# Kernel tuning notes

Hardware: AMD Instinct MI355X
Metric: run time of the kernel (lower is better)

## Reference

```python
import jax, jax.numpy as jnp
import numpy as np

EMBED_DIM = 1024
NUM_HEADS = 16
HEAD_DIM = EMBED_DIM // NUM_HEADS


def setup_inputs() -> dict:
    key = jax.random.key(0)
    ks = jax.random.split(key, 10)
    B, T, E = 2, 2048, EMBED_DIM

    def xavier(k, shape):
        fan_in, fan_out = shape[1], shape[0]
        limit = (6.0 / (fan_in + fan_out)) ** 0.5
        return jax.random.uniform(k, shape, jnp.float32, -limit, limit)

    return {
        "query": jax.random.normal(ks[0], (B, T, E), jnp.float32),
        "key": jax.random.normal(ks[1], (B, T, E), jnp.float32),
        "value": jax.random.normal(ks[2], (B, T, E), jnp.float32),
        "Wq": xavier(ks[3], (E, E)),
        "Wk": xavier(ks[4], (E, E)),
        "Wv": xavier(ks[5], (E, E)),
        "bq": jnp.zeros((E,), jnp.float32),
        "bk": jnp.zeros((E,), jnp.float32),
        "bv": jnp.zeros((E,), jnp.float32),
        "Wo": xavier(ks[6], (E, E)),
        "bo": jnp.zeros((E,), jnp.float32),
    }


def reference(query, key, value, Wq, Wk, Wv, bq, bk, bv, Wo, bo):
    B, Tq, E = query.shape
    Tk = key.shape[1]
    H, hd = NUM_HEADS, HEAD_DIM

    # In-projections (nn.Linear convention: x @ W.T + b)
    q = query @ Wq.T + bq  # (B, Tq, E)
    k = key @ Wk.T + bk    # (B, Tk, E)
    v = value @ Wv.T + bv  # (B, Tk, E)

    # Split heads -> (B, H, T, hd)
    q = q.reshape(B, Tq, H, hd).transpose(0, 2, 1, 3)
    k = k.reshape(B, Tk, H, hd).transpose(0, 2, 1, 3)
    v = v.reshape(B, Tk, H, hd).transpose(0, 2, 1, 3)

    # Scaled dot-product attention (dropout=0, no mask)
    scores = jnp.einsum("bhqd,bhkd->bhqk", q, k) / jnp.sqrt(jnp.float32(hd))
    attn = jax.nn.softmax(scores, axis=-1)
    out = jnp.einsum("bhqk,bhkd->bhqd", attn, v)  # (B, H, Tq, hd)

    # Merge heads and out-projection
    out = out.transpose(0, 2, 1, 3).reshape(B, Tq, E)
    return out @ Wo.T + bo
```

## Files before the change

kernel.cpp:

```cpp
#include <hip/hip_runtime.h>
#include <hip/hip_bf16.h>
#include <stdint.h>


#define NHEAD 16
#define SEQT  2048
#define EDIM  1024
#define HD    64
#define MB    2
#define MTOT  (MB*SEQT)

typedef __attribute__((ext_vector_type(4))) float f32x4;
typedef __attribute__((ext_vector_type(8))) short s16x8;

typedef const __attribute__((address_space(1))) void* GPtr;
typedef __attribute__((address_space(3))) void* LPtr;

__device__ __forceinline__ ushort f2bf(float f) {
    uint32_t u = __float_as_uint(f);
    u += 0x7FFF + ((u >> 16) & 1);
    return (ushort)(u >> 16);
}
__device__ __forceinline__ float bf2f(ushort h) {
    return __uint_as_float(((uint32_t)h) << 16);
}

__device__ __forceinline__ void gload_lds16(const void* g, void* l) {
    __builtin_amdgcn_global_load_lds((GPtr)g, (LPtr)l, 16, 0, 0);
}

__global__ void cvt_kernel(const float* __restrict__ src, ushort* __restrict__ dst, int n4) {
    int idx = blockIdx.x * blockDim.x + threadIdx.x;
    int stride = gridDim.x * blockDim.x;
    for (int i = idx; i < n4; i += stride) {
        float4 v = reinterpret_cast<const float4*>(src)[i];
        ushort4 o;
        o.x = f2bf(v.x); o.y = f2bf(v.y); o.z = f2bf(v.z); o.w = f2bf(v.w);
        reinterpret_cast<ushort4*>(dst)[i] = o;
    }
}

template<int OUTMODE>
__device__ __forceinline__ void gemm_body(const ushort* __restrict__ A,
                                          const ushort* __restrict__ W,
                                          const float* __restrict__ bias,
                                          void* __restrict__ out)
{
    const int K = 1024, N = 1024;
    __shared__ ushort As[128 * 32];
    __shared__ ushort Bs[128 * 32];

    const int tid  = threadIdx.x;
    const int lane = tid & 63;
    const int wid  = tid >> 6;
    const int wr = wid >> 1, wc = wid & 1;
    const int bm = blockIdx.y, bn = blockIdx.x;

    f32x4 acc[4][4];
#pragma unroll
    for (int i = 0; i < 4; i++)
#pragma unroll
        for (int j = 0; j < 4; j++) acc[i][j] = (f32x4){0.f, 0.f, 0.f, 0.f};

    const ushort* Abase = A + (size_t)(bm * 128) * K;
    const ushort* Wbase = W + (size_t)(bn * 128) * K;
    ushort* AsW = As + wid * 512;
    ushort* BsW = Bs + wid * 512;
    const int srow = tid >> 2;
    const int scol = (tid & 3) * 8;

    const int afoff = (wr * 64 + (lane & 15)) * 32 + (lane >> 4) * 8;
    const int bfoff = (wc * 64 + (lane & 15)) * 32 + (lane >> 4) * 8;

    for (int k0 = 0; k0 < K; k0 += 32) {
#pragma unroll
        for (int j = 0; j < 2; j++) {
            gload_lds16(Abase + (size_t)(j * 64 + srow) * K + k0 + scol, AsW + j * 2048);
            gload_lds16(Wbase + (size_t)(j * 64 + srow) * K + k0 + scol, BsW + j * 2048);
        }
        __syncthreads();

        s16x8 af[4], bf[4];
#pragma unroll
        for (int i = 0; i < 4; i++)
            af[i] = *reinterpret_cast<const s16x8*>(&As[afoff + i * 16 * 32]);
#pragma unroll
        for (int j = 0; j < 4; j++)
            bf[j] = *reinterpret_cast<const s16x8*>(&Bs[bfoff + j * 16 * 32]);
#pragma unroll
        for (int i = 0; i < 4; i++)
#pragma unroll
            for (int j = 0; j < 4; j++)
                acc[i][j] = __builtin_amdgcn_mfma_f32_16x16x32_bf16(af[i], bf[j], acc[i][j], 0, 0, 0);
        __syncthreads();
    }

    const int orow0 = bm * 128 + wr * 64 + (lane >> 4) * 4;
    const int ocol0 = bn * 128 + wc * 64 + (lane & 15);
#pragma unroll
    for (int i = 0; i < 4; i++) {
#pragma unroll
        for (int j = 0; j < 4; j++) {
            int col = ocol0 + j * 16;
            float bv = bias[col];
#pragma unroll
            for (int r = 0; r < 4; r++) {
                int row = orow0 + i * 16 + r;
                float v = acc[i][j][r] + bv;
                if (OUTMODE == 0) {
                    int b = row >> 11, t = row & (SEQT - 1);
                    int h = col >> 6,  d = col & 63;
                    ((ushort*)out)[(((size_t)b * NHEAD + h) * SEQT + t) * HD + d] = f2bf(v);
                } else {
                    ((float*)out)[(size_t)row * N + col] = v;
                }
            }
        }
    }
}

__global__ __launch_bounds__(256, 2)
void proj3_kernel(const ushort* xq, const ushort* xk, const ushort* xv,
                  const ushort* wq, const ushort* wk, const ushort* wv,
                  const float* bq, const float* bk, const float* bv,
                  ushort* oq, ushort* ok, ushort* ov)
{
    int z = blockIdx.z;
    const ushort* A = (z == 0) ? xq : (z == 1) ? xk : xv;
    const ushort* W = (z == 0) ? wq : (z == 1) ? wk : wv;
    const float* bi = (z == 0) ? bq : (z == 1) ? bk : bv;
    ushort* o       = (z == 0) ? oq : (z == 1) ? ok : ov;
    gemm_body<0>(A, W, bi, o);
}

__global__ __launch_bounds__(256, 2)
void oproj_kernel(const ushort* __restrict__ A, const ushort* __restrict__ W,
                  const float* __restrict__ bias, float* __restrict__ out)
{
    gemm_body<1>(A, W, bias, out);
}

#define KBLK 64
#define DPAD 72

__global__ __launch_bounds__(512, 2)
void attn_kernel(const ushort* __restrict__ Qg, const ushort* __restrict__ Kg,
                 const ushort* __restrict__ Vg, ushort* __restrict__ Og)
{
    __shared__ ushort Ks[KBLK][DPAD];
    __shared__ ushort Vts[HD][DPAD];
    __shared__ ushort Ps[8][16][DPAD];

    const int tid  = threadIdx.x;
    const int lane = tid & 63;
    const int wid  = tid >> 6;
    const int bh   = blockIdx.y;
    const int q0   = blockIdx.x * 128;

    const ushort* Qb = Qg + (size_t)bh * SEQT * HD;
    const ushort* Kb = Kg + (size_t)bh * SEQT * HD;
    const ushort* Vb = Vg + (size_t)bh * SEQT * HD;

    const float CS = 0.18033688011112042f;
    s16x8 qf[2];
    {
        int r  = q0 + wid * 16 + (lane & 15);
        int d0 = (lane >> 4) * 8;
#pragma unroll
        for (int kk = 0; kk < 2; kk++) {
            s16x8 raw = *reinterpret_cast<const s16x8*>(&Qb[(size_t)r * HD + kk * 32 + d0]);
            s16x8 sc;
#pragma unroll
            for (int i = 0; i < 8; i++) sc[i] = (short)f2bf(bf2f((ushort)raw[i]) * CS);
            qf[kk] = sc;
        }
    }

    f32x4 o[4];
#pragma unroll
    for (int i = 0; i < 4; i++) o[i] = (f32x4){0.f, 0.f, 0.f, 0.f};
    float mrow[4], lrow[4];
#pragma unroll
    for (int r = 0; r < 4; r++) { mrow[r] = -1e30f; lrow[r] = 0.f; }

    for (int t0 = 0; t0 < SEQT; t0 += KBLK) {
        {
            int e  = tid * 8;
            int kr = e >> 6;
            int dc = e & 63;
            s16x8 kv = *reinterpret_cast<const s16x8*>(&Kb[(size_t)(t0 + kr) * HD + dc]);
            *reinterpret_cast<s16x8*>(&Ks[kr][dc]) = kv;
            s16x8 vv = *reinterpret_cast<const s16x8*>(&Vb[(size_t)(t0 + kr) * HD + dc]);
#pragma unroll
            for (int i = 0; i < 8; i++) {
                int ii = (i + tid) & 7;
                Vts[dc + ii][kr] = (ushort)vv[ii];
            }
        }
        __syncthreads();

        f32x4 s[4];
#pragma unroll
        for (int nj = 0; nj < 4; nj++) {
            f32x4 a = (f32x4){0.f, 0.f, 0.f, 0.f};
#pragma unroll
            for (int kk = 0; kk < 2; kk++) {
                s16x8 kf = *reinterpret_cast<const s16x8*>(
                    &Ks[nj * 16 + (lane & 15)][kk * 32 + (lane >> 4) * 8]);
                a = __builtin_amdgcn_mfma_f32_16x16x32_bf16(qf[kk], kf, a, 0, 0, 0);
            }
            s[nj] = a;
        }

        float alpha[4], rsum[4];
#pragma unroll
        for (int r = 0; r < 4; r++) {
            float m0 = fmaxf(fmaxf(s[0][r], s[1][r]), fmaxf(s[2][r], s[3][r]));
#pragma unroll
            for (int off = 1; off < 16; off <<= 1) m0 = fmaxf(m0, __shfl_xor(m0, off));
            float mn = fmaxf(mrow[r], m0);
            alpha[r] = exp2f(mrow[r] - mn);
            mrow[r] = mn;
            rsum[r] = 0.f;
        }
        const int prow = (lane >> 4) * 4;
        const int pcol = lane & 15;
#pragma unroll
        for (int nj = 0; nj < 4; nj++) {
#pragma unroll
            for (int r = 0; r < 4; r++) {
                float p = exp2f(s[nj][r] - mrow[r]);
                rsum[r] += p;
                Ps[wid][prow + r][nj * 16 + pcol] = f2bf(p);
            }
        }
#pragma unroll
        for (int r = 0; r < 4; r++) {
            float su = rsum[r];
#pragma unroll
            for (int off = 1; off < 16; off <<= 1) su += __shfl_xor(su, off);
            lrow[r] = lrow[r] * alpha[r] + su;
        }
#pragma unroll
        for (int dj = 0; dj < 4; dj++)
#pragma unroll
            for (int r = 0; r < 4; r++) o[dj][r] *= alpha[r];

        s16x8 pa[2];
#pragma unroll
        for (int kk = 0; kk < 2; kk++)
            pa[kk] = *reinterpret_cast<const s16x8*>(
                &Ps[wid][lane & 15][kk * 32 + (lane >> 4) * 8]);
#pragma unroll
        for (int dj = 0; dj < 4; dj++) {
#pragma unroll
            for (int kk = 0; kk < 2; kk++) {
                s16x8 vf = *reinterpret_cast<const s16x8*>(
                    &Vts[dj * 16 + (lane & 15)][kk * 32 + (lane >> 4) * 8]);
                o[dj] = __builtin_amdgcn_mfma_f32_16x16x32_bf16(pa[kk], vf, o[dj], 0, 0, 0);
            }
        }
        __syncthreads();
    }

    const int b = bh >> 4, h = bh & 15;
    const int trow = q0 + wid * 16 + (lane >> 4) * 4;
#pragma unroll
    for (int dj = 0; dj < 4; dj++) {
        int col = h * 64 + dj * 16 + (lane & 15);
#pragma unroll
        for (int r = 0; r < 4; r++) {
            float v = o[dj][r] / lrow[r];
            Og[((size_t)b * SEQT + trow + r) * EDIM + col] = f2bf(v);
        }
    }
}

extern "C" void kernel_launch(void* const* d_in, const int* in_sizes, int n_in,
                              void* d_out, int out_size, void* d_ws, size_t ws_size,
                              hipStream_t stream)
{
    const float* query = (const float*)d_in[0];
    const float* key   = (const float*)d_in[1];
    const float* value = (const float*)d_in[2];
    const float* Wq    = (const float*)d_in[3];
    const float* Wk    = (const float*)d_in[4];
    const float* Wv    = (const float*)d_in[5];
    const float* bq    = (const float*)d_in[6];
    const float* bk    = (const float*)d_in[7];
    const float* bv    = (const float*)d_in[8];
    const float* Wo    = (const float*)d_in[9];
    const float* bo    = (const float*)d_in[10];
    float* out = (float*)d_out;

    const size_t NX = (size_t)MTOT * EDIM;
    const size_t NW = (size_t)EDIM * EDIM;
    ushort* ws = (ushort*)d_ws;
    ushort* xq = ws;
    ushort* xk = xq + NX;
    ushort* xv = xk + NX;
    ushort* wq = xv + NX;
    ushort* wk = wq + NW;
    ushort* wv = wk + NW;
    ushort* wo = wv + NW;
    ushort* qb = wo + NW;
    ushort* kb = qb + NX;
    ushort* vb = kb + NX;
    ushort* ao = vb + NX;

    const int n4x = (int)(NX / 4), n4w = (int)(NW / 4);
    cvt_kernel<<<dim3(1024), 256, 0, stream>>>(query, xq, n4x);
    cvt_kernel<<<dim3(1024), 256, 0, stream>>>(key,   xk, n4x);
    cvt_kernel<<<dim3(1024), 256, 0, stream>>>(value, xv, n4x);
    cvt_kernel<<<dim3(512),  256, 0, stream>>>(Wq, wq, n4w);
    cvt_kernel<<<dim3(512),  256, 0, stream>>>(Wk, wk, n4w);
    cvt_kernel<<<dim3(512),  256, 0, stream>>>(Wv, wv, n4w);
    cvt_kernel<<<dim3(512),  256, 0, stream>>>(Wo, wo, n4w);

    proj3_kernel<<<dim3(8, 32, 3), 256, 0, stream>>>(xq, xk, xv, wq, wk, wv,
                                                     bq, bk, bv, qb, kb, vb);

    attn_kernel<<<dim3(SEQT / 128, MB * NHEAD), 512, 0, stream>>>(qb, kb, vb, ao);

    oproj_kernel<<<dim3(8, 32), 256, 0, stream>>>(ao, wo, bo, out);
}
```

Measured before the change: 326.0 us.

## Rewrite attention with 32x32 MFMA, pre-transposed swizzled V/K, async double-buffered LDS

The V projection is now computed as W·Xᵀ so it is written already transposed, and K and Vᵀ are stored with XOR-swizzled layouts. This removes the per-tile LDS transpose of V in the attention loop. The attention kernel switches to 32x32x16 MFMA with 256 threads. It streams K/V tiles into double-buffered LDS via global_load_lds and keeps P in registers, using packed bf16 conversion and cross-half shuffles instead of an LDS round trip. Output goes through LDS for coalesced 16-byte stores, at the cost of splitting the fused QKV projection launch into three launches.

```diff
diff --git a/kernel.cpp b/kernel.cpp
--- a/kernel.cpp
+++ b/kernel.cpp
@@ -10,23 +10,28 @@
 #define MB    2
 #define MTOT  (MB*SEQT)
 
-typedef __attribute__((ext_vector_type(4))) float f32x4;
-typedef __attribute__((ext_vector_type(8))) short s16x8;
+typedef __attribute__((ext_vector_type(4)))  float f32x4;
+typedef __attribute__((ext_vector_type(16))) float f32x16;
+typedef __attribute__((ext_vector_type(8)))  short s16x8;
 
 typedef const __attribute__((address_space(1))) void* GPtr;
 typedef __attribute__((address_space(3))) void* LPtr;
 
-__device__ __forceinline__ ushort f2bf(float f) {
+static __device__ __forceinline__ ushort f2bf(float f) {
     uint32_t u = __float_as_uint(f);
     u += 0x7FFF + ((u >> 16) & 1);
     return (ushort)(u >> 16);
 }
-__device__ __forceinline__ float bf2f(ushort h) {
+static __device__ __forceinline__ float bf2f(ushort h) {
     return __uint_as_float(((uint32_t)h) << 16);
 }
-
-__device__ __forceinline__ void gload_lds16(const void* g, void* l) {
+static __device__ __forceinline__ void gload_lds16(const void* g, void* l) {
     __builtin_amdgcn_global_load_lds((GPtr)g, (LPtr)l, 16, 0, 0);
+}
+static __device__ __forceinline__ uint cvt_pk_bf16(float lo, float hi) {
+    uint r;
+    asm("v_cvt_pk_bf16_f32 %0, %1, %2" : "=v"(r) : "v"(lo), "v"(hi));
+    return r;
 }
 
 __global__ void cvt_kernel(const float* __restrict__ src, ushort* __restrict__ dst, int n4) {
@@ -102,17 +107,27 @@
 #pragma unroll
         for (int j = 0; j < 4; j++) {
             int col = ocol0 + j * 16;
-            float bv = bias[col];
 #pragma unroll
             for (int r = 0; r < 4; r++) {
                 int row = orow0 + i * 16 + r;
+                float bv = (OUTMODE == 2) ? bias[row] : bias[col];
                 float v = acc[i][j][r] + bv;
                 if (OUTMODE == 0) {
                     int b = row >> 11, t = row & (SEQT - 1);
                     int h = col >> 6,  d = col & 63;
                     ((ushort*)out)[(((size_t)b * NHEAD + h) * SEQT + t) * HD + d] = f2bf(v);
+                } else if (OUTMODE == 1) {
+                    ((float*)out)[(size_t)row * N + col] = v;
+                } else if (OUTMODE == 2) {
+                    int h = row >> 6, d = row & 63;
+                    int b = col >> 11, t = col & (SEQT - 1);
+                    int tsw = (t & ~63) | ((t & 63) ^ ((d & 7) << 3));
+                    ((ushort*)out)[(((size_t)b * NHEAD + h) * HD + d) * SEQT + tsw] = f2bf(v);
                 } else {
-                    ((float*)out)[(size_t)row * N + col] = v;
+                    int b = row >> 11, t = row & (SEQT - 1);
+                    int h = col >> 6,  d = col & 63;
+                    int dsw = d ^ ((t & 7) << 3);
+                    ((ushort*)out)[(((size_t)b * NHEAD + h) * SEQT + t) * HD + dsw] = f2bf(v);
                 }
             }
         }
@@ -120,159 +135,178 @@
 }
 
 __global__ __launch_bounds__(256, 2)
-void proj3_kernel(const ushort* xq, const ushort* xk, const ushort* xv,
-                  const ushort* wq, const ushort* wk, const ushort* wv,
-                  const float* bq, const float* bk, const float* bv,
-                  ushort* oq, ushort* ok, ushort* ov)
-{
-    int z = blockIdx.z;
-    const ushort* A = (z == 0) ? xq : (z == 1) ? xk : xv;
-    const ushort* W = (z == 0) ? wq : (z == 1) ? wk : wv;
-    const float* bi = (z == 0) ? bq : (z == 1) ? bk : bv;
-    ushort* o       = (z == 0) ? oq : (z == 1) ? ok : ov;
+void projQ_kernel(const ushort* A, const ushort* W, const float* bi, ushort* o) {
     gemm_body<0>(A, W, bi, o);
 }
-
+__global__ __launch_bounds__(256, 2)
+void projK_kernel(const ushort* A, const ushort* W, const float* bi, ushort* o) {
+    gemm_body<3>(A, W, bi, o);
+}
+__global__ __launch_bounds__(256, 2)
+void projVT_kernel(const ushort* A, const ushort* W, const float* bi, ushort* o) {
+    gemm_body<2>(A, W, bi, o);
+}
 __global__ __launch_bounds__(256, 2)
 void oproj_kernel(const ushort* __restrict__ A, const ushort* __restrict__ W,
-                  const float* __restrict__ bias, float* __restrict__ out)
+                  const float* __restrict__ bias, float* __restrict__ out) {
+    gemm_body<1>(A, W, bias, out);
+}
+
+#define KBLK 64
+#define NT (SEQT / KBLK)
+
+__global__ __launch_bounds__(256)
+void attn_kernel(const ushort* __restrict__ Qg, const ushort* __restrict__ Kg,
+                 const ushort* __restrict__ Vtg, ushort* __restrict__ Og)
 {
-    gemm_body<1>(A, W, bias, out);
-}
-
-#define KBLK 64
-#define DPAD 72
-
-__global__ __launch_bounds__(512, 2)
-void attn_kernel(const ushort* __restrict__ Qg, const ushort* __restrict__ Kg,
-                 const ushort* __restrict__ Vg, ushort* __restrict__ Og)
-{
-    __shared__ ushort Ks[KBLK][DPAD];
-    __shared__ ushort Vts[HD][DPAD];
-    __shared__ ushort Ps[8][16][DPAD];
+    __shared__ ushort Ks[2][KBLK * HD];
+    __shared__ ushort Vs[2][HD * KBLK];
 
     const int tid  = threadIdx.x;
     const int lane = tid & 63;
     const int wid  = tid >> 6;
+    const int g    = lane >> 5;
+    const int qc   = lane & 31;
     const int bh   = blockIdx.y;
-    const int q0   = blockIdx.x * 128;
-
-    const ushort* Qb = Qg + (size_t)bh * SEQT * HD;
-    const ushort* Kb = Kg + (size_t)bh * SEQT * HD;
-    const ushort* Vb = Vg + (size_t)bh * SEQT * HD;
+    const int q0   = blockIdx.x * 128 + wid * 32;
+
+    const ushort* Kp = Kg  + (size_t)bh * SEQT * HD;
+    const ushort* Vp = Vtg + (size_t)bh * HD * SEQT;
 
     const float CS = 0.18033688011112042f;
-    s16x8 qf[2];
+    s16x8 qf[4];
     {
-        int r  = q0 + wid * 16 + (lane & 15);
-        int d0 = (lane >> 4) * 8;
-#pragma unroll
-        for (int kk = 0; kk < 2; kk++) {
-            s16x8 raw = *reinterpret_cast<const s16x8*>(&Qb[(size_t)r * HD + kk * 32 + d0]);
+        const ushort* Qp = Qg + ((size_t)bh * SEQT + q0 + qc) * HD;
+#pragma unroll
+        for (int kst = 0; kst < 4; kst++) {
+            s16x8 raw = *reinterpret_cast<const s16x8*>(Qp + kst * 16 + g * 8);
             s16x8 sc;
 #pragma unroll
-            for (int i = 0; i < 8; i++) sc[i] = (short)f2bf(bf2f((ushort)raw[i]) * CS);
-            qf[kk] = sc;
-        }
-    }
-
-    f32x4 o[4];
-#pragma unroll
-    for (int i = 0; i < 4; i++) o[i] = (f32x4){0.f, 0.f, 0.f, 0.f};
-    float mrow[4], lrow[4];
-#pragma unroll
-    for (int r = 0; r < 4; r++) { mrow[r] = -1e30f; lrow[r] = 0.f; }
-
-    for (int t0 = 0; t0 < SEQT; t0 += KBLK) {
-        {
-            int e  = tid * 8;
-            int kr = e >> 6;
-            int dc = e & 63;
-            s16x8 kv = *reinterpret_cast<const s16x8*>(&Kb[(size_t)(t0 + kr) * HD + dc]);
-            *reinterpret_cast<s16x8*>(&Ks[kr][dc]) = kv;
-            s16x8 vv = *reinterpret_cast<const s16x8*>(&Vb[(size_t)(t0 + kr) * HD + dc]);
-#pragma unroll
-            for (int i = 0; i < 8; i++) {
-                int ii = (i + tid) & 7;
-                Vts[dc + ii][kr] = (ushort)vv[ii];
+            for (int j = 0; j < 8; j++) sc[j] = (short)f2bf(bf2f((ushort)raw[j]) * CS);
+            qf[kst] = sc;
+        }
+    }
+
+    f32x16 oa[2];
+#pragma unroll
+    for (int mt = 0; mt < 2; mt++)
+#pragma unroll
+        for (int r = 0; r < 16; r++) oa[mt][r] = 0.f;
+    float mrow = -1e30f, lrow = 0.f;
+
+#define STAGE(buf, t0)                                                               \
+    do {                                                                             \
+        _Pragma("unroll")                                                            \
+        for (int c = 0; c < 2; c++) {                                                \
+            int i = c * 256 + tid;                                                   \
+            gload_lds16(Kp + (size_t)((t0) + (i >> 3)) * HD + (i & 7) * 8,           \
+                        &Ks[buf][(c * 256 + wid * 64) * 8]);                         \
+            gload_lds16(Vp + (size_t)(i >> 3) * SEQT + (t0) + (i & 7) * 8,           \
+                        &Vs[buf][(c * 256 + wid * 64) * 8]);                         \
+        }                                                                            \
+    } while (0)
+
+    STAGE(0, 0);
+    __syncthreads();
+    int cur = 0;
+
+    for (int t = 0; t < NT; t++) {
+        if (t + 1 < NT) STAGE(cur ^ 1, (t + 1) * KBLK);
+        const ushort* Kb = Ks[cur];
+        const ushort* Vb = Vs[cur];
+
+        f32x16 sa[2];
+#pragma unroll
+        for (int mt = 0; mt < 2; mt++) {
+            f32x16 a;
+#pragma unroll
+            for (int r = 0; r < 16; r++) a[r] = 0.f;
+            const int key = mt * 32 + qc;
+#pragma unroll
+            for (int kst = 0; kst < 4; kst++) {
+                int dsw = (kst * 16 + g * 8) ^ ((key & 7) << 3);
+                s16x8 kf = *reinterpret_cast<const s16x8*>(Kb + key * HD + dsw);
+                a = __builtin_amdgcn_mfma_f32_32x32x16_bf16(kf, qf[kst], a, 0, 0, 0);
             }
+            sa[mt] = a;
+        }
+
+        float mx = sa[0][0];
+#pragma unroll
+        for (int r = 1; r < 16; r++) mx = fmaxf(mx, sa[0][r]);
+#pragma unroll
+        for (int r = 0; r < 16; r++) mx = fmaxf(mx, sa[1][r]);
+        mx = fmaxf(mx, __shfl_xor(mx, 32));
+        float mn = fmaxf(mrow, mx);
+        float alpha = exp2f(mrow - mn);
+        mrow = mn;
+        float rs = 0.f;
+#pragma unroll
+        for (int mt = 0; mt < 2; mt++)
+#pragma unroll
+            for (int r = 0; r < 16; r++) {
+                float p = exp2f(sa[mt][r] - mn);
+                sa[mt][r] = p;
+                rs += p;
+            }
+        rs += __shfl_xor(rs, 32);
+        lrow = lrow * alpha + rs;
+#pragma unroll
+        for (int mt = 0; mt < 2; mt++)
+#pragma unroll
+            for (int r = 0; r < 16; r++) oa[mt][r] *= alpha;
+
+        uint pk[2][8];
+#pragma unroll
+        for (int aa = 0; aa < 2; aa++)
+#pragma unroll
+            for (int p = 0; p < 8; p++)
+                pk[aa][p] = cvt_pk_bf16(sa[aa][2 * p], sa[aa][2 * p + 1]);
+
+#pragma unroll
+        for (int kst = 0; kst < 4; kst++) {
+            const int aa = kst >> 1;
+            const int b4 = (kst & 1) * 4;
+            uint s0 = g ? pk[aa][b4 + 0] : pk[aa][b4 + 2];
+            uint s1 = g ? pk[aa][b4 + 1] : pk[aa][b4 + 3];
+            uint r0 = __shfl_xor(s0, 32);
+            uint r1 = __shfl_xor(s1, 32);
+            union { uint u[4]; s16x8 v; } pf;
+            pf.u[0] = g ? r0 : pk[aa][b4 + 0];
+            pf.u[1] = g ? r1 : pk[aa][b4 + 1];
+            pf.u[2] = g ? pk[aa][b4 + 2] : r0;
+            pf.u[3] = g ? pk[aa][b4 + 3] : r1;
+#pragma unroll
+            for (int mt = 0; mt < 2; mt++) {
+                const int d = mt * 32 + qc;
+                int ksw = (kst * 16 + g * 8) ^ ((d & 7) << 3);
+                s16x8 vf = *reinterpret_cast<const s16x8*>(Vb + d * KBLK + ksw);
+                oa[mt] = __builtin_amdgcn_mfma_f32_32x32x16_bf16(vf, pf.v, oa[mt], 0, 0, 0);
+            }
         }
         __syncthreads();
-
-        f32x4 s[4];
-#pragma unroll
-        for (int nj = 0; nj < 4; nj++) {
-            f32x4 a = (f32x4){0.f, 0.f, 0.f, 0.f};
-#pragma unroll
-            for (int kk = 0; kk < 2; kk++) {
-                s16x8 kf = *reinterpret_cast<const s16x8*>(
-                    &Ks[nj * 16 + (lane & 15)][kk * 32 + (lane >> 4) * 8]);
-                a = __builtin_amdgcn_mfma_f32_16x16x32_bf16(qf[kk], kf, a, 0, 0, 0);
-            }
-            s[nj] = a;
-        }
-
-        float alpha[4], rsum[4];
-#pragma unroll
-        for (int r = 0; r < 4; r++) {
-            float m0 = fmaxf(fmaxf(s[0][r], s[1][r]), fmaxf(s[2][r], s[3][r]));
-#pragma unroll
-            for (int off = 1; off < 16; off <<= 1) m0 = fmaxf(m0, __shfl_xor(m0, off));
-            float mn = fmaxf(mrow[r], m0);
-            alpha[r] = exp2f(mrow[r] - mn);
-            mrow[r] = mn;
-            rsum[r] = 0.f;
-        }
-        const int prow = (lane >> 4) * 4;
-        const int pcol = lane & 15;
-#pragma unroll
-        for (int nj = 0; nj < 4; nj++) {
-#pragma unroll
-            for (int r = 0; r < 4; r++) {
-                float p = exp2f(s[nj][r] - mrow[r]);
-                rsum[r] += p;
-                Ps[wid][prow + r][nj * 16 + pcol] = f2bf(p);
-            }
-        }
-#pragma unroll
-        for (int r = 0; r < 4; r++) {
-            float su = rsum[r];
-#pragma unroll
-            for (int off = 1; off < 16; off <<= 1) su += __shfl_xor(su, off);
-            lrow[r] = lrow[r] * alpha[r] + su;
-        }
-#pragma unroll
-        for (int dj = 0; dj < 4; dj++)
-#pragma unroll
-            for (int r = 0; r < 4; r++) o[dj][r] *= alpha[r];
-
-        s16x8 pa[2];
-#pragma unroll
-        for (int kk = 0; kk < 2; kk++)
-            pa[kk] = *reinterpret_cast<const s16x8*>(
-                &Ps[wid][lane & 15][kk * 32 + (lane >> 4) * 8]);
-#pragma unroll
-        for (int dj = 0; dj < 4; dj++) {
-#pragma unroll
-            for (int kk = 0; kk < 2; kk++) {
-                s16x8 vf = *reinterpret_cast<const s16x8*>(
-                    &Vts[dj * 16 + (lane & 15)][kk * 32 + (lane >> 4) * 8]);
-                o[dj] = __builtin_amdgcn_mfma_f32_16x16x32_bf16(pa[kk], vf, o[dj], 0, 0, 0);
-            }
-        }
-        __syncthreads();
-    }
-
+        cur ^= 1;
+    }
+
+    float inv = 1.0f / lrow;
+    ushort* Ob = &Ks[0][0] + wid * 2048;
+#pragma unroll
+    for (int mt = 0; mt < 2; mt++)
+#pragma unroll
+        for (int p = 0; p < 8; p++) {
+            int d = mt * 32 + ((2 * p) & 3) + 8 * (p >> 1) + 4 * g;
+            uint v = cvt_pk_bf16(oa[mt][2 * p] * inv, oa[mt][2 * p + 1] * inv);
+            *reinterpret_cast<uint*>(Ob + qc * HD + (d ^ ((qc & 7) << 3))) = v;
+        }
+    __syncthreads();
     const int b = bh >> 4, h = bh & 15;
-    const int trow = q0 + wid * 16 + (lane >> 4) * 4;
-#pragma unroll
-    for (int dj = 0; dj < 4; dj++) {
-        int col = h * 64 + dj * 16 + (lane & 15);
-#pragma unroll
-        for (int r = 0; r < 4; r++) {
-            float v = o[dj][r] / lrow[r];
-            Og[((size_t)b * SEQT + trow + r) * EDIM + col] = f2bf(v);
-        }
+    const int qr = lane >> 1, dh = (lane & 1) * 32;
+    ushort* dst = Og + ((size_t)b * SEQT + q0 + qr) * EDIM + h * HD + dh;
+    const ushort* src = Ob + qr * HD;
+#pragma unroll
+    for (int c = 0; c < 4; c++) {
+        int d0 = (dh + c * 8) ^ ((qr & 7) << 3);
+        *reinterpret_cast<s16x8*>(dst + c * 8) = *reinterpret_cast<const s16x8*>(src + d0);
     }
 }
 
@@ -296,17 +330,17 @@
     const size_t NX = (size_t)MTOT * EDIM;
     const size_t NW = (size_t)EDIM * EDIM;
     ushort* ws = (ushort*)d_ws;
-    ushort* xq = ws;
-    ushort* xk = xq + NX;
-    ushort* xv = xk + NX;
-    ushort* wq = xv + NX;
-    ushort* wk = wq + NW;
-    ushort* wv = wk + NW;
-    ushort* wo = wv + NW;
-    ushort* qb = wo + NW;
-    ushort* kb = qb + NX;
-    ushort* vb = kb + NX;
-    ushort* ao = vb + NX;
+    ushort* xq  = ws;
+    ushort* xk  = xq + NX;
+    ushort* xv  = xk + NX;
+    ushort* wq  = xv + NX;
+    ushort* wk  = wq + NW;
+    ushort* wv  = wk + NW;
+    ushort* wo  = wv + NW;
+    ushort* qb  = wo + NW;
+    ushort* kb  = qb + NX;
+    ushort* vtb = kb + NX;
+    ushort* ao  = vtb + NX;
 
     const int n4x = (int)(NX / 4), n4w = (int)(NW / 4);
     cvt_kernel<<<dim3(1024), 256, 0, stream>>>(query, xq, n4x);
@@ -317,10 +351,11 @@
     cvt_kernel<<<dim3(512),  256, 0, stream>>>(Wv, wv, n4w);
     cvt_kernel<<<dim3(512),  256, 0, stream>>>(Wo, wo, n4w);
 
-    proj3_kernel<<<dim3(8, 32, 3), 256, 0, stream>>>(xq, xk, xv, wq, wk, wv,
-                                                     bq, bk, bv, qb, kb, vb);
-
-    attn_kernel<<<dim3(SEQT / 128, MB * NHEAD), 512, 0, stream>>>(qb, kb, vb, ao);
+    projQ_kernel <<<dim3(8, 32),  256, 0, stream>>>(xq, wq, bq, qb);
+    projK_kernel <<<dim3(8, 32),  256, 0, stream>>>(xk, wk, bk, kb);
+    projVT_kernel<<<dim3(32, 8),  256, 0, stream>>>(wv, xv, bv, vtb);
+
+    attn_kernel<<<dim3(SEQT / 128, MB * NHEAD), 256, 0, stream>>>(qb, kb, vtb, ao);
 
     oproj_kernel<<<dim3(8, 32), 256, 0, stream>>>(ao, wo, bo, out);
 }
```

After: 298.6 us. 1.09x faster.
